# Performance work log

Measured on AMD Instinct MI355X. Metric: run time of the kernel, lower is better.

The kernel has to match this reference:

```python
import jax, jax.numpy as jnp
import numpy as np

B, N, D = 256, 512, 128   # meta_batch, num_sample, feat_dim; in_c = 2*D = 256, base_c = 128
EPS_L1 = 1e-12
EPS_BN = 1e-5
NEG_SLOPE = 0.01


def setup_inputs() -> dict:
    key = jax.random.key(0)
    ks = jax.random.split(key, 6)
    return {
        "distribution_edge": jax.random.uniform(ks[0], (B, N, N), dtype=jnp.float32),
        "instance_edge": jax.random.uniform(ks[1], (B, N, N), dtype=jnp.float32),
        "point_node": jax.random.normal(ks[2], (B, N, D), dtype=jnp.float32),
        "W1": jax.random.normal(ks[3], (2 * D, 2 * D), dtype=jnp.float32) * 0.05,  # Conv2d 1x1: (out_c=base_c*2, in_c)
        "g1": jnp.ones((2 * D,), jnp.float32),
        "b1": jnp.zeros((2 * D,), jnp.float32),
        "W2": jax.random.normal(ks[4], (D, 2 * D), dtype=jnp.float32) * 0.05,     # Conv2d 1x1: (out_c=base_c, base_c*2)
        "g2": jnp.ones((D,), jnp.float32),
        "b2": jnp.zeros((D,), jnp.float32),
    }


def _l1_normalize(x):
    # F.normalize(x, p=1, dim=-1): x / max(sum(|x|, -1), 1e-12)
    return x / jnp.clip(jnp.sum(jnp.abs(x), axis=-1, keepdims=True), EPS_L1, None)


def _bn_lrelu(x, g, b):
    # x: (B, C, N); BatchNorm2d training-mode stats over (batch, spatial), biased var
    mean = jnp.mean(x, axis=(0, 2), keepdims=True)
    var = jnp.var(x, axis=(0, 2), keepdims=True)
    y = (x - mean) * jax.lax.rsqrt(var + EPS_BN) * g[None, :, None] + b[None, :, None]
    return jnp.where(y >= 0, y, NEG_SLOPE * y)


def reference(distribution_edge, instance_edge, point_node, W1, g1, b1, W2, g2, b2):
    n = point_node.shape[1]
    diag_mask = 1.0 - jnp.eye(n, dtype=point_node.dtype)  # broadcasts over meta_batch
    edge_feat = _l1_normalize(distribution_edge * diag_mask)
    aggr_feat = jnp.einsum('bij,bjd->bid', edge_feat, point_node)
    edge_instance = _l1_normalize(instance_edge * diag_mask)
    aggr_instance = jnp.einsum('bij,bjd->bid', edge_instance, point_node)
    x = jnp.concatenate([aggr_feat, aggr_instance], axis=-1)  # (B, N, 2D)
    x = jnp.swapaxes(x, 1, 2)                                  # (B, 2D, N)
    h = _bn_lrelu(jnp.einsum('oc,bcn->bon', W1, x), g1, b1)    # 1x1 conv, no bias
    h = _bn_lrelu(jnp.einsum('oc,bcn->bon', W2, h), g2, b2)
    return jnp.swapaxes(h, 1, 2)                               # (B, N, base_c)
```

## Files before the change

kernel.cpp:

```cpp
#include <hip/hip_runtime.h>
#include <hip/hip_bf16.h>
#include <string.h>

#define BB 256
#define NNS 512
#define DDF 128
#define CC1 256
#define CC2 128
#define NPOS (BB * NNS)

typedef __attribute__((ext_vector_type(4))) float f32x4;
typedef __attribute__((ext_vector_type(8))) short bf16x8;

__device__ __forceinline__ short f2bf(float f) {
    __hip_bfloat16 h = __float2bfloat16(f);
    short s;
    __builtin_memcpy(&s, &h, 2);
    return s;
}
__device__ __forceinline__ float bf2f(short s) {
    unsigned int u = ((unsigned int)(unsigned short)s) << 16;
    float f;
    __builtin_memcpy(&f, &u, 4);
    return f;
}
__device__ __forceinline__ unsigned int pk2bf(float a, float b) {
    float2 t; t.x = a; t.y = b;
    __hip_bfloat162 h = __float22bfloat162_rn(t);
    unsigned int u;
    __builtin_memcpy(&u, &h, 4);
    return u;
}

__device__ __forceinline__ void gload_lds16(const void* g, void* l) {
    __builtin_amdgcn_global_load_lds(
        (const __attribute__((address_space(1))) unsigned int*)g,
        (__attribute__((address_space(3))) unsigned int*)l, 16, 0, 0);
}

#define MFMA16(a, b, c) __builtin_amdgcn_mfma_f32_16x16x32_bf16(a, b, c, 0, 0, 0)

__global__ void prep_kernel(const float* __restrict__ W1, const float* __restrict__ W2,
                            short* __restrict__ W1b, short* __restrict__ W2b,
                            float* __restrict__ stats) {
    int idx = blockIdx.x * 256 + threadIdx.x;
    if (idx < CC1 * CC1) W1b[idx] = f2bf(W1[idx]);
    if (idx < CC2 * CC1) W2b[idx] = f2bf(W2[idx]);
    if (idx < 1536) stats[idx] = 0.0f;
}

__global__ __launch_bounds__(256) void transposeP_kernel(const float* __restrict__ P,
                                                         short* __restrict__ PT) {
    __shared__ float tp[64 * 132];
    int b = blockIdx.x >> 3;
    int j0 = (blockIdx.x & 7) * 64;
    int t = threadIdx.x;
    const float* Pb = P + ((size_t)b * NNS + j0) * DDF;
    int jr = t >> 5, dc = (t & 31) * 4;
#pragma unroll
    for (int p = 0; p < 8; ++p) {
        int j = p * 8 + jr;
        float4 v = *reinterpret_cast<const float4*>(&Pb[(size_t)j * DDF + dc]);
        *reinterpret_cast<float4*>(&tp[j * 132 + dc]) = v;
    }
    __syncthreads();
    int jo = t & 7;
#pragma unroll
    for (int p = 0; p < 4; ++p) {
        int d = p * 32 + (t >> 3);
        bf16x8 v;
#pragma unroll
        for (int s = 0; s < 8; ++s) v[s] = f2bf(tp[(jo * 8 + s) * 132 + d]);
        *reinterpret_cast<bf16x8*>(&PT[((size_t)(b * DDF + d)) * NNS + j0 + jo * 8]) = v;
    }
}

__global__ __launch_bounds__(256) void gemm1_kernel(const float* __restrict__ dE,
                                                    const float* __restrict__ iE,
                                                    const short* __restrict__ PT,
                                                    short* __restrict__ X) {
    __shared__ __align__(16) float tA[2][4096];
    int bid = blockIdx.x;
    int mtb = bid & 3;
    int e = (bid >> 2) & 1;
    int b = bid >> 3;
    const float* E = (e == 0 ? dE : iE) + (size_t)b * (NNS * NNS);
    const short* PTb = PT + (size_t)b * (DDF * NNS);

    int tid = threadIdx.x;
    int lane = tid & 63, w = tid >> 6;
    int quad = lane >> 4, lr = lane & 15;
    int mh = w >> 1, nh = w & 1;
    int mbase = mtb * 128;
    int mwave = mh * 64;

    int srow[4], scol[4];
#pragma unroll
    for (int i = 0; i < 4; ++i) {
        int rl = i * 32 + (tid >> 3);
        srow[i] = rl;
        scol[i] = (tid & 7) ^ (rl & 7);
    }

    f32x4 zero = {0.f, 0.f, 0.f, 0.f};
    f32x4 acc[4][4];
#pragma unroll
    for (int a = 0; a < 4; ++a)
#pragma unroll
        for (int c = 0; c < 4; ++c) acc[a][c] = zero;
    float rs[4] = {0.f, 0.f, 0.f, 0.f};

#pragma unroll
    for (int i = 0; i < 4; ++i)
        gload_lds16(&E[(size_t)(mbase + srow[i]) * NNS + scol[i] * 4],
                    (char*)&tA[0][0] + i * 4096 + w * 1024);
    __syncthreads();

    for (int kk = 0; kk < 16; ++kk) {
        const float* cur = &tA[kk & 1][0];
        if (kk < 15) {
            float* nxt = &tA[(kk + 1) & 1][0];
            int kc = (kk + 1) * 32;
#pragma unroll
            for (int i = 0; i < 4; ++i)
                gload_lds16(&E[(size_t)(mbase + srow[i]) * NNS + kc + scol[i] * 4],
                            (char*)nxt + i * 4096 + w * 1024);
        }
        int k0 = kk * 32 + quad * 8;
        bf16x8 bfr[4];
#pragma unroll
        for (int nt = 0; nt < 4; ++nt) {
            int n = nh * 64 + nt * 16 + lr;
            bfr[nt] = *reinterpret_cast<const bf16x8*>(&PTb[(size_t)n * NNS + k0]);
        }
#pragma unroll
        for (int mt = 0; mt < 4; ++mt) {
            int rl = mwave + mt * 16 + lr;
            int i = mbase + rl;
            int sw = rl & 7;
            int s0 = rl * 8 + ((quad * 2) ^ sw);
            int s1 = rl * 8 + ((quad * 2 + 1) ^ sw);
            float4 v0 = *reinterpret_cast<const float4*>(&cur[s0 * 4]);
            float4 v1 = *reinterpret_cast<const float4*>(&cur[s1 * 4]);
            float a8[8] = {v0.x, v0.y, v0.z, v0.w, v1.x, v1.y, v1.z, v1.w};
#pragma unroll
            for (int tt = 0; tt < 8; ++tt)
                if (k0 + tt == i) a8[tt] = 0.0f;
#pragma unroll
            for (int tt = 0; tt < 8; ++tt) rs[mt] += fabsf(a8[tt]);
            union { bf16x8 v; unsigned int u[4]; } af;
#pragma unroll
            for (int tt = 0; tt < 4; ++tt) af.u[tt] = pk2bf(a8[2 * tt], a8[2 * tt + 1]);
#pragma unroll
            for (int nt = 0; nt < 4; ++nt) acc[mt][nt] = MFMA16(af.v, bfr[nt], acc[mt][nt]);
        }
        __syncthreads();
    }

    float inv[4];
#pragma unroll
    for (int mt = 0; mt < 4; ++mt) {
        float s = rs[mt];
        s += __shfl_xor(s, 16, 64);
        s += __shfl_xor(s, 32, 64);
        inv[mt] = 1.0f / fmaxf(s, 1e-12f);
    }
#pragma unroll
    for (int mt = 0; mt < 4; ++mt) {
        float ir[4];
#pragma unroll
        for (int r = 0; r < 4; ++r) ir[r] = __shfl(inv[mt], quad * 4 + r, 64);
#pragma unroll
        for (int nt = 0; nt < 4; ++nt) {
            int col = e * 128 + nh * 64 + nt * 16 + lr;
#pragma unroll
            for (int r = 0; r < 4; ++r) {
                int row = mbase + mwave + mt * 16 + quad * 4 + r;
                X[((size_t)b * NNS + row) * CC1 + col] = f2bf(acc[mt][nt][r] * ir[r]);
            }
        }
    }
}

__global__ __launch_bounds__(512) void gemm2_kernel(const short* __restrict__ X,
                                                    const short* __restrict__ W1b,
                                                    short* __restrict__ Y1,
                                                    float* __restrict__ sum1,
                                                    float* __restrict__ sumsq1) {
    __shared__ __align__(16) short tA[2][4096];
    int pbase = blockIdx.x * 128;
    int tid = threadIdx.x;
    int lane = tid & 63, w = tid >> 6;
    int quad = lane >> 4, lr = lane & 15;
    int mh = w >> 2, nh = w & 3;

    int spair = tid >> 3;
    int sl3 = (tid & 7) ^ (spair & 7);
    int srow = spair * 2 + (sl3 >> 2);
    int scol = sl3 & 3;

    f32x4 zero = {0.f, 0.f, 0.f, 0.f};
    f32x4 acc[4][4];
#pragma unroll
    for (int a = 0; a < 4; ++a)
#pragma unroll
        for (int c = 0; c < 4; ++c) acc[a][c] = zero;

    gload_lds16(&X[(size_t)(pbase + srow) * CC1 + scol * 8], (char*)&tA[0][0] + w * 1024);
    __syncthreads();

    for (int kk = 0; kk < 8; ++kk) {
        const short* cur = &tA[kk & 1][0];
        if (kk < 7)
            gload_lds16(&X[(size_t)(pbase + srow) * CC1 + (kk + 1) * 32 + scol * 8],
                        (char*)&tA[(kk + 1) & 1][0] + w * 1024);
        int k0 = kk * 32 + quad * 8;
        bf16x8 bfr[4];
#pragma unroll
        for (int nt = 0; nt < 4; ++nt) {
            int o = nh * 64 + nt * 16 + lr;
            bfr[nt] = *reinterpret_cast<const bf16x8*>(&W1b[(size_t)o * CC1 + k0]);
        }
#pragma unroll
        for (int mt = 0; mt < 4; ++mt) {
            int rl = mh * 64 + mt * 16 + lr;
            int pair = rl >> 1;
            int s3 = ((rl & 1) << 2) | quad;
            int phys = pair * 8 + (s3 ^ (pair & 7));
            bf16x8 af = *reinterpret_cast<const bf16x8*>(&cur[phys * 8]);
#pragma unroll
            for (int nt = 0; nt < 4; ++nt) acc[mt][nt] = MFMA16(af, bfr[nt], acc[mt][nt]);
        }
        __syncthreads();
    }
#pragma unroll
    for (int nt = 0; nt < 4; ++nt) {
        int o = nh * 64 + nt * 16 + lr;
        float s = 0.f, q = 0.f;
#pragma unroll
        for (int mt = 0; mt < 4; ++mt)
#pragma unroll
            for (int r = 0; r < 4; ++r) {
                float v = acc[mt][nt][r];
                s += v;
                q += v * v;
            }
        s += __shfl_xor(s, 16, 64); s += __shfl_xor(s, 32, 64);
        q += __shfl_xor(q, 16, 64); q += __shfl_xor(q, 32, 64);
        if (lane < 16) {
            atomicAdd(&sum1[o], s);
            atomicAdd(&sumsq1[o], q);
        }
#pragma unroll
        for (int mt = 0; mt < 4; ++mt)
#pragma unroll
            for (int r = 0; r < 4; ++r) {
                int pos = pbase + mh * 64 + mt * 16 + quad * 4 + r;
                Y1[(size_t)pos * CC1 + o] = f2bf(acc[mt][nt][r]);
            }
    }
}

__global__ void finalize_kernel(const float* __restrict__ sum, const float* __restrict__ sumsq,
                                const float* __restrict__ g, const float* __restrict__ b,
                                float* __restrict__ scale, float* __restrict__ shift, int C) {
    int i = threadIdx.x;
    if (i < C) {
        const float invM = 1.0f / (float)NPOS;
        float m = sum[i] * invM;
        float v = sumsq[i] * invM - m * m;
        float s = g[i] * rsqrtf(v + 1e-5f);
        scale[i] = s;
        shift[i] = b[i] - m * s;
    }
}

__global__ __launch_bounds__(256) void gemm3_kernel(const short* __restrict__ Y1,
                                                    const short* __restrict__ W2b,
                                                    const float* __restrict__ scale1,
                                                    const float* __restrict__ shift1,
                                                    float* __restrict__ Y2,
                                                    float* __restrict__ sum2,
                                                    float* __restrict__ sumsq2) {
    __shared__ __align__(16) short tA[2][4096];
    __shared__ __align__(16) float ssc[CC1];
    __shared__ __align__(16) float ssh[CC1];
    ssc[threadIdx.x] = scale1[threadIdx.x];
    ssh[threadIdx.x] = shift1[threadIdx.x];

    int pbase = blockIdx.x * 128;
    int tid = threadIdx.x;
    int lane = tid & 63, w = tid >> 6;
    int quad = lane >> 4, lr = lane & 15;
    int mh = w >> 1, nh = w & 1;

    int srow[2], scol[2];
#pragma unroll
    for (int i = 0; i < 2; ++i) {
        int slot = i * 256 + tid;
        int pair = slot >> 3;
        int s3 = (slot & 7) ^ (pair & 7);
        srow[i] = pair * 2 + (s3 >> 2);
        scol[i] = s3 & 3;
    }

    f32x4 zero = {0.f, 0.f, 0.f, 0.f};
    f32x4 acc[4][4];
#pragma unroll
    for (int a = 0; a < 4; ++a)
#pragma unroll
        for (int c = 0; c < 4; ++c) acc[a][c] = zero;

#pragma unroll
    for (int i = 0; i < 2; ++i)
        gload_lds16(&Y1[(size_t)(pbase + srow[i]) * CC1 + scol[i] * 8],
                    (char*)&tA[0][0] + i * 4096 + w * 1024);
    __syncthreads();

    for (int kk = 0; kk < 8; ++kk) {
        const short* cur = &tA[kk & 1][0];
        if (kk < 7) {
#pragma unroll
            for (int i = 0; i < 2; ++i)
                gload_lds16(&Y1[(size_t)(pbase + srow[i]) * CC1 + (kk + 1) * 32 + scol[i] * 8],
                            (char*)&tA[(kk + 1) & 1][0] + i * 4096 + w * 1024);
        }
        int k0 = kk * 32 + quad * 8;
        bf16x8 bfr[4];
#pragma unroll
        for (int nt = 0; nt < 4; ++nt) {
            int o = nh * 64 + nt * 16 + lr;
            bfr[nt] = *reinterpret_cast<const bf16x8*>(&W2b[(size_t)o * CC1 + k0]);
        }
        float4 sc0 = *reinterpret_cast<const float4*>(&ssc[k0]);
        float4 sc1 = *reinterpret_cast<const float4*>(&ssc[k0 + 4]);
        float4 sh0 = *reinterpret_cast<const float4*>(&ssh[k0]);
        float4 sh1 = *reinterpret_cast<const float4*>(&ssh[k0 + 4]);
        float scv[8] = {sc0.x, sc0.y, sc0.z, sc0.w, sc1.x, sc1.y, sc1.z, sc1.w};
        float shv[8] = {sh0.x, sh0.y, sh0.z, sh0.w, sh1.x, sh1.y, sh1.z, sh1.w};
#pragma unroll
        for (int mt = 0; mt < 4; ++mt) {
            int rl = mh * 64 + mt * 16 + lr;
            int pair = rl >> 1;
            int s3 = ((rl & 1) << 2) | quad;
            int phys = pair * 8 + (s3 ^ (pair & 7));
            bf16x8 raw = *reinterpret_cast<const bf16x8*>(&cur[phys * 8]);
            union { bf16x8 v; unsigned int u[4]; } af;
#pragma unroll
            for (int tt = 0; tt < 4; ++tt) {
                float va = bf2f(raw[2 * tt]) * scv[2 * tt] + shv[2 * tt];
                va = fmaxf(va, 0.01f * va);
                float vb = bf2f(raw[2 * tt + 1]) * scv[2 * tt + 1] + shv[2 * tt + 1];
                vb = fmaxf(vb, 0.01f * vb);
                af.u[tt] = pk2bf(va, vb);
            }
#pragma unroll
            for (int nt = 0; nt < 4; ++nt) acc[mt][nt] = MFMA16(af.v, bfr[nt], acc[mt][nt]);
        }
        __syncthreads();
    }
#pragma unroll
    for (int nt = 0; nt < 4; ++nt) {
        int o = nh * 64 + nt * 16 + lr;
        float s = 0.f, q = 0.f;
#pragma unroll
        for (int mt = 0; mt < 4; ++mt)
#pragma unroll
            for (int r = 0; r < 4; ++r) {
                float v = acc[mt][nt][r];
                s += v;
                q += v * v;
            }
        s += __shfl_xor(s, 16, 64); s += __shfl_xor(s, 32, 64);
        q += __shfl_xor(q, 16, 64); q += __shfl_xor(q, 32, 64);
        if (lane < 16) {
            atomicAdd(&sum2[o], s);
            atomicAdd(&sumsq2[o], q);
        }
#pragma unroll
        for (int mt = 0; mt < 4; ++mt)
#pragma unroll
            for (int r = 0; r < 4; ++r) {
                int pos = pbase + mh * 64 + mt * 16 + quad * 4 + r;
                Y2[(size_t)pos * CC2 + o] = acc[mt][nt][r];
            }
    }
}

__global__ void apply2_kernel(const float* __restrict__ Y2, const float* __restrict__ scale2,
                              const float* __restrict__ shift2, float* __restrict__ out) {
    size_t gid = (size_t)blockIdx.x * 256 + threadIdx.x;
    size_t base = gid * 4;
    float4 y = *reinterpret_cast<const float4*>(&Y2[base]);
    int o = (int)(base & 127);
    float4 sc = *reinterpret_cast<const float4*>(&scale2[o]);
    float4 sh = *reinterpret_cast<const float4*>(&shift2[o]);
    float4 t;
    t.x = y.x * sc.x + sh.x; t.x = fmaxf(t.x, 0.01f * t.x);
    t.y = y.y * sc.y + sh.y; t.y = fmaxf(t.y, 0.01f * t.y);
    t.z = y.z * sc.z + sh.z; t.z = fmaxf(t.z, 0.01f * t.z);
    t.w = y.w * sc.w + sh.w; t.w = fmaxf(t.w, 0.01f * t.w);
    *reinterpret_cast<float4*>(&out[base]) = t;
}

extern "C" void kernel_launch(void* const* d_in, const int* in_sizes, int n_in,
                              void* d_out, int out_size, void* d_ws, size_t ws_size,
                              hipStream_t stream) {
    const float* dE = (const float*)d_in[0];
    const float* iE = (const float*)d_in[1];
    const float* P  = (const float*)d_in[2];
    const float* W1 = (const float*)d_in[3];
    const float* g1 = (const float*)d_in[4];
    const float* b1 = (const float*)d_in[5];
    const float* W2 = (const float*)d_in[6];
    const float* g2 = (const float*)d_in[7];
    const float* b2 = (const float*)d_in[8];
    float* out = (float*)d_out;
    char* ws = (char*)d_ws;

    short* PT  = (short*)(ws + 0);
    short* X   = (short*)(ws + 33554432);
    short* Y1  = (short*)(ws + 100663296);
    float* Y2  = (float*)(ws + 33554432);
    short* W1b = (short*)(ws + 167772160);
    short* W2b = (short*)(ws + 167903232);
    float* st  = (float*)(ws + 167968768);
    float* sum1 = st,        * sumsq1 = st + 256, * scale1 = st + 512,  * shift1 = st + 768;
    float* sum2 = st + 1024, * sumsq2 = st + 1152, * scale2 = st + 1280, * shift2 = st + 1408;

    prep_kernel<<<256, 256, 0, stream>>>(W1, W2, W1b, W2b, st);
    transposeP_kernel<<<2048, 256, 0, stream>>>(P, PT);
    gemm1_kernel<<<2048, 256, 0, stream>>>(dE, iE, PT, X);
    gemm2_kernel<<<1024, 512, 0, stream>>>(X, W1b, Y1, sum1, sumsq1);
    finalize_kernel<<<1, 256, 0, stream>>>(sum1, sumsq1, g1, b1, scale1, shift1, CC1);
    gemm3_kernel<<<1024, 256, 0, stream>>>(Y1, W2b, scale1, shift1, Y2, sum2, sumsq2);
    finalize_kernel<<<1, 128, 0, stream>>>(sum2, sumsq2, g2, b2, scale2, shift2, CC2);
    apply2_kernel<<<16384, 256, 0, stream>>>(Y2, scale2, shift2, out);
}
```

Before: 781.4 us.

## Replace LDS staging with direct register-prefetched global loads in all GEMM kernels

Removes the shared-memory double buffering (global_load_lds plus barriers) from the three GEMM kernels. Each wave now loads its A fragments straight from global memory into registers, prefetching one k-step ahead. In gemm1 the wave tiling changes to 32 rows by all 128 columns per wave, and the diagonal mask check is limited to the single k-step that holds the diagonal. The aim is to cut LDS traffic and sync overhead, at the cost of uncoalesced strided global reads and more register pressure from the wider accumulator set. A missing barrier after the scale/shift LDS fill is also added.

Result: slower. 866.3 us (+10.9%).

```diff
diff --git a/kernel.cpp b/kernel.cpp
--- a/kernel.cpp
+++ b/kernel.cpp
@@ -30,12 +30,6 @@
     unsigned int u;
     __builtin_memcpy(&u, &h, 4);
     return u;
-}
-
-__device__ __forceinline__ void gload_lds16(const void* g, void* l) {
-    __builtin_amdgcn_global_load_lds(
-        (const __attribute__((address_space(1))) unsigned int*)g,
-        (__attribute__((address_space(3))) unsigned int*)l, 16, 0, 0);
 }
 
 #define MFMA16(a, b, c) __builtin_amdgcn_mfma_f32_16x16x32_bf16(a, b, c, 0, 0, 0)
@@ -79,7 +73,6 @@
                                                     const float* __restrict__ iE,
                                                     const short* __restrict__ PT,
                                                     short* __restrict__ X) {
-    __shared__ __align__(16) float tA[2][4096];
     int bid = blockIdx.x;
     int mtb = bid & 3;
     int e = (bid >> 2) & 1;
@@ -90,92 +83,81 @@
     int tid = threadIdx.x;
     int lane = tid & 63, w = tid >> 6;
     int quad = lane >> 4, lr = lane & 15;
-    int mh = w >> 1, nh = w & 1;
-    int mbase = mtb * 128;
-    int mwave = mh * 64;
-
-    int srow[4], scol[4];
-#pragma unroll
-    for (int i = 0; i < 4; ++i) {
-        int rl = i * 32 + (tid >> 3);
-        srow[i] = rl;
-        scol[i] = (tid & 7) ^ (rl & 7);
-    }
+    int rbase = mtb * 128 + w * 32;
+
+    const float* Ap[2];
+#pragma unroll
+    for (int mt = 0; mt < 2; ++mt)
+        Ap[mt] = E + (size_t)(rbase + mt * 16 + lr) * NNS + quad * 8;
+    const short* Bp[8];
+#pragma unroll
+    for (int nt = 0; nt < 8; ++nt)
+        Bp[nt] = PTb + (size_t)(nt * 16 + lr) * NNS + quad * 8;
 
     f32x4 zero = {0.f, 0.f, 0.f, 0.f};
-    f32x4 acc[4][4];
-#pragma unroll
-    for (int a = 0; a < 4; ++a)
-#pragma unroll
-        for (int c = 0; c < 4; ++c) acc[a][c] = zero;
-    float rs[4] = {0.f, 0.f, 0.f, 0.f};
-
-#pragma unroll
-    for (int i = 0; i < 4; ++i)
-        gload_lds16(&E[(size_t)(mbase + srow[i]) * NNS + scol[i] * 4],
-                    (char*)&tA[0][0] + i * 4096 + w * 1024);
-    __syncthreads();
-
+    f32x4 acc[2][8];
+#pragma unroll
+    for (int a = 0; a < 2; ++a)
+#pragma unroll
+        for (int c = 0; c < 8; ++c) acc[a][c] = zero;
+    float rs[2] = {0.f, 0.f};
+
+    float4 pa0[2], pa1[2];
+#pragma unroll
+    for (int mt = 0; mt < 2; ++mt) {
+        pa0[mt] = *reinterpret_cast<const float4*>(Ap[mt]);
+        pa1[mt] = *reinterpret_cast<const float4*>(Ap[mt] + 4);
+    }
+    int kkd = rbase >> 5;
+
+#pragma unroll 2
     for (int kk = 0; kk < 16; ++kk) {
-        const float* cur = &tA[kk & 1][0];
-        if (kk < 15) {
-            float* nxt = &tA[(kk + 1) & 1][0];
-            int kc = (kk + 1) * 32;
-#pragma unroll
-            for (int i = 0; i < 4; ++i)
-                gload_lds16(&E[(size_t)(mbase + srow[i]) * NNS + kc + scol[i] * 4],
-                            (char*)nxt + i * 4096 + w * 1024);
-        }
-        int k0 = kk * 32 + quad * 8;
-        bf16x8 bfr[4];
-#pragma unroll
-        for (int nt = 0; nt < 4; ++nt) {
-            int n = nh * 64 + nt * 16 + lr;
-            bfr[nt] = *reinterpret_cast<const bf16x8*>(&PTb[(size_t)n * NNS + k0]);
-        }
-#pragma unroll
-        for (int mt = 0; mt < 4; ++mt) {
-            int rl = mwave + mt * 16 + lr;
-            int i = mbase + rl;
-            int sw = rl & 7;
-            int s0 = rl * 8 + ((quad * 2) ^ sw);
-            int s1 = rl * 8 + ((quad * 2 + 1) ^ sw);
-            float4 v0 = *reinterpret_cast<const float4*>(&cur[s0 * 4]);
-            float4 v1 = *reinterpret_cast<const float4*>(&cur[s1 * 4]);
+        bf16x8 bv[8];
+#pragma unroll
+        for (int nt = 0; nt < 8; ++nt)
+            bv[nt] = *reinterpret_cast<const bf16x8*>(Bp[nt] + kk * 32);
+#pragma unroll
+        for (int mt = 0; mt < 2; ++mt) {
+            float4 v0 = pa0[mt], v1 = pa1[mt];
+            if (kk < 15) {
+                pa0[mt] = *reinterpret_cast<const float4*>(Ap[mt] + (kk + 1) * 32);
+                pa1[mt] = *reinterpret_cast<const float4*>(Ap[mt] + (kk + 1) * 32 + 4);
+            }
             float a8[8] = {v0.x, v0.y, v0.z, v0.w, v1.x, v1.y, v1.z, v1.w};
-#pragma unroll
-            for (int tt = 0; tt < 8; ++tt)
-                if (k0 + tt == i) a8[tt] = 0.0f;
-#pragma unroll
-            for (int tt = 0; tt < 8; ++tt) rs[mt] += fabsf(a8[tt]);
+            if (kk == kkd) {
+                int t = (mt << 4) + lr;
+#pragma unroll
+                for (int tt = 0; tt < 8; ++tt)
+                    if (quad * 8 + tt == t) a8[tt] = 0.0f;
+            }
+            float s = rs[mt];
+#pragma unroll
+            for (int tt = 0; tt < 8; ++tt) s += fabsf(a8[tt]);
+            rs[mt] = s;
             union { bf16x8 v; unsigned int u[4]; } af;
 #pragma unroll
             for (int tt = 0; tt < 4; ++tt) af.u[tt] = pk2bf(a8[2 * tt], a8[2 * tt + 1]);
 #pragma unroll
-            for (int nt = 0; nt < 4; ++nt) acc[mt][nt] = MFMA16(af.v, bfr[nt], acc[mt][nt]);
-        }
-        __syncthreads();
-    }
-
-    float inv[4];
-#pragma unroll
-    for (int mt = 0; mt < 4; ++mt) {
+            for (int nt = 0; nt < 8; ++nt)
+                acc[mt][nt] = MFMA16(af.v, bv[nt], acc[mt][nt]);
+        }
+    }
+
+#pragma unroll
+    for (int mt = 0; mt < 2; ++mt) {
         float s = rs[mt];
         s += __shfl_xor(s, 16, 64);
         s += __shfl_xor(s, 32, 64);
-        inv[mt] = 1.0f / fmaxf(s, 1e-12f);
-    }
-#pragma unroll
-    for (int mt = 0; mt < 4; ++mt) {
+        float inv = 1.0f / fmaxf(s, 1e-12f);
         float ir[4];
 #pragma unroll
-        for (int r = 0; r < 4; ++r) ir[r] = __shfl(inv[mt], quad * 4 + r, 64);
-#pragma unroll
-        for (int nt = 0; nt < 4; ++nt) {
-            int col = e * 128 + nh * 64 + nt * 16 + lr;
+        for (int r = 0; r < 4; ++r) ir[r] = __shfl(inv, quad * 4 + r, 64);
+#pragma unroll
+        for (int nt = 0; nt < 8; ++nt) {
+            int col = e * 128 + nt * 16 + lr;
 #pragma unroll
             for (int r = 0; r < 4; ++r) {
-                int row = mbase + mwave + mt * 16 + quad * 4 + r;
+                int row = rbase + mt * 16 + quad * 4 + r;
                 X[((size_t)b * NNS + row) * CC1 + col] = f2bf(acc[mt][nt][r] * ir[r]);
             }
         }
@@ -187,17 +169,20 @@
                                                     short* __restrict__ Y1,
                                                     float* __restrict__ sum1,
                                                     float* __restrict__ sumsq1) {
-    __shared__ __align__(16) short tA[2][4096];
     int pbase = blockIdx.x * 128;
     int tid = threadIdx.x;
     int lane = tid & 63, w = tid >> 6;
     int quad = lane >> 4, lr = lane & 15;
     int mh = w >> 2, nh = w & 3;
 
-    int spair = tid >> 3;
-    int sl3 = (tid & 7) ^ (spair & 7);
-    int srow = spair * 2 + (sl3 >> 2);
-    int scol = sl3 & 3;
+    const short* Ap[4];
+#pragma unroll
+    for (int mt = 0; mt < 4; ++mt)
+        Ap[mt] = X + (size_t)(pbase + mh * 64 + mt * 16 + lr) * CC1 + quad * 8;
+    const short* Bp[4];
+#pragma unroll
+    for (int nt = 0; nt < 4; ++nt)
+        Bp[nt] = W1b + (size_t)(nh * 64 + nt * 16 + lr) * CC1 + quad * 8;
 
     f32x4 zero = {0.f, 0.f, 0.f, 0.f};
     f32x4 acc[4][4];
@@ -206,32 +191,23 @@
 #pragma unroll
         for (int c = 0; c < 4; ++c) acc[a][c] = zero;
 
-    gload_lds16(&X[(size_t)(pbase + srow) * CC1 + scol * 8], (char*)&tA[0][0] + w * 1024);
-    __syncthreads();
-
+    bf16x8 pa[4];
+#pragma unroll
+    for (int mt = 0; mt < 4; ++mt) pa[mt] = *reinterpret_cast<const bf16x8*>(Ap[mt]);
+
+#pragma unroll 2
     for (int kk = 0; kk < 8; ++kk) {
-        const short* cur = &tA[kk & 1][0];
-        if (kk < 7)
-            gload_lds16(&X[(size_t)(pbase + srow) * CC1 + (kk + 1) * 32 + scol * 8],
-                        (char*)&tA[(kk + 1) & 1][0] + w * 1024);
-        int k0 = kk * 32 + quad * 8;
-        bf16x8 bfr[4];
-#pragma unroll
-        for (int nt = 0; nt < 4; ++nt) {
-            int o = nh * 64 + nt * 16 + lr;
-            bfr[nt] = *reinterpret_cast<const bf16x8*>(&W1b[(size_t)o * CC1 + k0]);
-        }
+        bf16x8 bv[4];
+#pragma unroll
+        for (int nt = 0; nt < 4; ++nt)
+            bv[nt] = *reinterpret_cast<const bf16x8*>(Bp[nt] + kk * 32);
 #pragma unroll
         for (int mt = 0; mt < 4; ++mt) {
-            int rl = mh * 64 + mt * 16 + lr;
-            int pair = rl >> 1;
-            int s3 = ((rl & 1) << 2) | quad;
-            int phys = pair * 8 + (s3 ^ (pair & 7));
-            bf16x8 af = *reinterpret_cast<const bf16x8*>(&cur[phys * 8]);
-#pragma unroll
-            for (int nt = 0; nt < 4; ++nt) acc[mt][nt] = MFMA16(af, bfr[nt], acc[mt][nt]);
-        }
-        __syncthreads();
+            bf16x8 av = pa[mt];
+            if (kk < 7) pa[mt] = *reinterpret_cast<const bf16x8*>(Ap[mt] + (kk + 1) * 32);
+#pragma unroll
+            for (int nt = 0; nt < 4; ++nt) acc[mt][nt] = MFMA16(av, bv[nt], acc[mt][nt]);
+        }
     }
 #pragma unroll
     for (int nt = 0; nt < 4; ++nt) {
@@ -282,11 +258,11 @@
                                                     float* __restrict__ Y2,
                                                     float* __restrict__ sum2,
                                                     float* __restrict__ sumsq2) {
-    __shared__ __align__(16) short tA[2][4096];
     __shared__ __align__(16) float ssc[CC1];
     __shared__ __align__(16) float ssh[CC1];
     ssc[threadIdx.x] = scale1[threadIdx.x];
     ssh[threadIdx.x] = shift1[threadIdx.x];
+    __syncthreads();
 
     int pbase = blockIdx.x * 128;
     int tid = threadIdx.x;
@@ -294,15 +270,14 @@
     int quad = lane >> 4, lr = lane & 15;
     int mh = w >> 1, nh = w & 1;
 
-    int srow[2], scol[2];
-#pragma unroll
-    for (int i = 0; i < 2; ++i) {
-        int slot = i * 256 + tid;
-        int pair = slot >> 3;
-        int s3 = (slot & 7) ^ (pair & 7);
-        srow[i] = pair * 2 + (s3 >> 2);
-        scol[i] = s3 & 3;
-    }
+    const short* Ap[4];
+#pragma unroll
+    for (int mt = 0; mt < 4; ++mt)
+        Ap[mt] = Y1 + (size_t)(pbase + mh * 64 + mt * 16 + lr) * CC1 + quad * 8;
+    const short* Bp[4];
+#pragma unroll
+    for (int nt = 0; nt < 4; ++nt)
+        Bp[nt] = W2b + (size_t)(nh * 64 + nt * 16 + lr) * CC1 + quad * 8;
 
     f32x4 zero = {0.f, 0.f, 0.f, 0.f};
     f32x4 acc[4][4];
@@ -311,27 +286,17 @@
 #pragma unroll
         for (int c = 0; c < 4; ++c) acc[a][c] = zero;
 
-#pragma unroll
-    for (int i = 0; i < 2; ++i)
-        gload_lds16(&Y1[(size_t)(pbase + srow[i]) * CC1 + scol[i] * 8],
-                    (char*)&tA[0][0] + i * 4096 + w * 1024);
-    __syncthreads();
-
+    bf16x8 pa[4];
+#pragma unroll
+    for (int mt = 0; mt < 4; ++mt) pa[mt] = *reinterpret_cast<const bf16x8*>(Ap[mt]);
+
+#pragma unroll 2
     for (int kk = 0; kk < 8; ++kk) {
-        const short* cur = &tA[kk & 1][0];
-        if (kk < 7) {
-#pragma unroll
-            for (int i = 0; i < 2; ++i)
-                gload_lds16(&Y1[(size_t)(pbase + srow[i]) * CC1 + (kk + 1) * 32 + scol[i] * 8],
-                            (char*)&tA[(kk + 1) & 1][0] + i * 4096 + w * 1024);
-        }
+        bf16x8 bv[4];
+#pragma unroll
+        for (int nt = 0; nt < 4; ++nt)
+            bv[nt] = *reinterpret_cast<const bf16x8*>(Bp[nt] + kk * 32);
         int k0 = kk * 32 + quad * 8;
-        bf16x8 bfr[4];
-#pragma unroll
-        for (int nt = 0; nt < 4; ++nt) {
-            int o = nh * 64 + nt * 16 + lr;
-            bfr[nt] = *reinterpret_cast<const bf16x8*>(&W2b[(size_t)o * CC1 + k0]);
-        }
         float4 sc0 = *reinterpret_cast<const float4*>(&ssc[k0]);
         float4 sc1 = *reinterpret_cast<const float4*>(&ssc[k0 + 4]);
         float4 sh0 = *reinterpret_cast<const float4*>(&ssh[k0]);
@@ -340,11 +305,8 @@
         float shv[8] = {sh0.x, sh0.y, sh0.z, sh0.w, sh1.x, sh1.y, sh1.z, sh1.w};
 #pragma unroll
         for (int mt = 0; mt < 4; ++mt) {
-            int rl = mh * 64 + mt * 16 + lr;
-            int pair = rl >> 1;
-            int s3 = ((rl & 1) << 2) | quad;
-            int phys = pair * 8 + (s3 ^ (pair & 7));
-            bf16x8 raw = *reinterpret_cast<const bf16x8*>(&cur[phys * 8]);
+            bf16x8 raw = pa[mt];
+            if (kk < 7) pa[mt] = *reinterpret_cast<const bf16x8*>(Ap[mt] + (kk + 1) * 32);
             union { bf16x8 v; unsigned int u[4]; } af;
 #pragma unroll
             for (int tt = 0; tt < 4; ++tt) {
@@ -355,9 +317,8 @@
                 af.u[tt] = pk2bf(va, vb);
             }
 #pragma unroll
-            for (int nt = 0; nt < 4; ++nt) acc[mt][nt] = MFMA16(af.v, bfr[nt], acc[mt][nt]);
-        }
-        __syncthreads();
+            for (int nt = 0; nt < 4; ++nt) acc[mt][nt] = MFMA16(af.v, bv[nt], acc[mt][nt]);
+        }
     }
 #pragma unroll
     for (int nt = 0; nt < 4; ++nt) {
```
